# Performance work log

Hardware: AMD Instinct MI355X
Metric: run time of the kernel (lower is better)

Reference implementation:

```python
import math
import jax, jax.numpy as jnp
import numpy as np

B, S, E = 2, 2048, 2048
H, D = 16, 128

def setup_inputs() -> dict:
    key = jax.random.key(0)
    ks = jax.random.split(key, 5)
    scale = 0.02
    return {
        "hidden_states": jax.random.normal(ks[0], (B, S, E), dtype=jnp.float32),
        "Wq": jax.random.normal(ks[1], (E, E), dtype=jnp.float32) * scale,
        "Wk": jax.random.normal(ks[2], (E, E), dtype=jnp.float32) * scale,
        "Wv": jax.random.normal(ks[3], (E, E), dtype=jnp.float32) * scale,
        "Wo": jax.random.normal(ks[4], (E, E), dtype=jnp.float32) * scale,
        "bo": jnp.zeros((E,), dtype=jnp.float32),
    }

def _split_heads(x):
    # [B,S,E] -> [B,H,S,D]
    b, s, _ = x.shape
    return x.reshape(b, s, H, D).transpose(0, 2, 1, 3)

def reference(hidden_states, Wq, Wk, Wv, Wo, bo):
    # torch nn.Linear: y = x @ W.T (q/k/v have no bias)
    q = _split_heads(hidden_states @ Wq.T)
    k = _split_heads(hidden_states @ Wk.T)
    v = _split_heads(hidden_states @ Wv.T)
    scores = jnp.einsum("bhqd,bhkd->bhqk", q, k) / math.sqrt(D)
    # causal mask: strictly-upper-triangular positions set to -inf ...
    causal = jnp.triu(jnp.ones((S, S), dtype=bool), k=1)
    scores = jnp.where(causal[None, None], -jnp.inf, scores)
    # ... then clamped to [-1e4, 1e4] (so masked logits become -10000, not -inf)
    scores = jnp.clip(scores, -10000.0, 10000.0)
    attn = jax.nn.softmax(scores, axis=-1)
    out = jnp.einsum("bhqk,bhkd->bhqd", attn, v)  # [B,H,S,D]
    out = out.transpose(0, 2, 1, 3).reshape(B, S, E)  # merge heads
    return out @ Wo.T + bo
```

## Files before the change

kernel.cpp:

```cpp
#include <hip/hip_runtime.h>
#include <hip/hip_bf16.h>
#include <stdint.h>
#include <math.h>

#define B_ 2
#define S_ 2048
#define E_ 2048
#define H_ 16
#define D_ 128
#define M_ (B_*S_)

typedef _Float16 half8 __attribute__((ext_vector_type(8)));
typedef _Float16 half4 __attribute__((ext_vector_type(4)));
typedef float    floatx4 __attribute__((ext_vector_type(4)));

__device__ __forceinline__ void async_copy16(const void* g, void* lds_base) {
    __builtin_amdgcn_global_load_lds(
        (__attribute__((address_space(1))) void*)(uintptr_t)g,
        (__attribute__((address_space(3))) void*)(uint32_t)(uintptr_t)lds_base,
        16, 0, 0);
}

__global__ __launch_bounds__(256) void cast_all(
    const float* __restrict__ X,  const float* __restrict__ Wq,
    const float* __restrict__ Wk, const float* __restrict__ Wv,
    const float* __restrict__ Wo,
    _Float16* __restrict__ Xh,  _Float16* __restrict__ Wqh,
    _Float16* __restrict__ Wkh, _Float16* __restrict__ Wvh,
    _Float16* __restrict__ Woh)
{
    const int z = blockIdx.z;
    const float* in; _Float16* out; size_t off = 0;
    switch (z) {
        case 0: in = X;  out = Xh;  off = 0;        break;
        case 1: in = X;  out = Xh;  off = 1048576;  break;
        case 2: in = Wq; out = Wqh; break;
        case 3: in = Wk; out = Wkh; break;
        case 4: in = Wv; out = Wvh; break;
        default: in = Wo; out = Woh; break;
    }
    size_t i = off + (size_t)blockIdx.x * 256 + threadIdx.x;
    floatx4 v = ((const floatx4*)in)[i];
    ((half4*)out)[i] = __builtin_convertvector(v, half4);
}

#define GBUF (128*64 + 256*64)

__device__ __forceinline__ void stage512(
    const _Float16* __restrict__ gsrc, int ldk,
    _Float16* lbase, int slot0, int wave, int lane)
{
    int slot = slot0 + wave*64 + lane;
    int row  = slot >> 3;
    int sg   = (slot & 7) ^ (row & 7);
    async_copy16(gsrc + (size_t)row * ldk + sg * 8,
                 lbase + (slot0 + wave*64) * 8);
}

template<bool BIAS, typename OutT, int NW, bool TRV>
__global__ __launch_bounds__(512, 2) void gemm_bt(
    const _Float16* __restrict__ A,
    const _Float16* __restrict__ W0, const _Float16* __restrict__ W1,
    const _Float16* __restrict__ W2,
    OutT* __restrict__ C0, OutT* __restrict__ C1, OutT* __restrict__ C2,
    const float* __restrict__ bias, int M, int N, int K)
{
    const _Float16* W = W0; OutT* C = C0;
    if (NW > 1) {
        if (blockIdx.y == 1) { W = W1; C = C1; }
        else if (blockIdx.y == 2) { W = W2; C = C2; }
    }
    __shared__ __align__(16) _Float16 sm[3 * GBUF];

    const int tid  = threadIdx.x;
    const int lane = tid & 63;
    const int wave = tid >> 6;
    const int wm = wave >> 2, wn = wave & 3;
    const int fr = lane & 15, fg = lane >> 4;

    const int bx = blockIdx.x;
    const int n_tile = bx & 7;
    const int m_tile = bx >> 3;
    const int m0 = m_tile * 128;
    const int n0 = n_tile * 256;

    const int NT = K >> 6;

#pragma unroll
    for (int pt = 0; pt < 2; ++pt) {
        _Float16* ab = &sm[pt * GBUF];
        _Float16* bb = ab + 128*64;
        const _Float16* Ag = A + (size_t)m0 * K + pt*64;
        const _Float16* Wg = W + (size_t)n0 * K + pt*64;
        stage512(Ag, K, ab, 0,    wave, lane);
        stage512(Ag, K, ab, 512,  wave, lane);
        stage512(Wg, K, bb, 0,    wave, lane);
        stage512(Wg, K, bb, 512,  wave, lane);
        stage512(Wg, K, bb, 1024, wave, lane);
        stage512(Wg, K, bb, 1536, wave, lane);
    }

    floatx4 acc[4][4] = {};

    for (int t = 0; t < NT; ++t) {
        if (t + 1 < NT) { __asm__ __volatile__("s_waitcnt vmcnt(6)" ::: "memory"); }
        else            { __asm__ __volatile__("s_waitcnt vmcnt(0)" ::: "memory"); }
        __builtin_amdgcn_sched_barrier(0);
        __builtin_amdgcn_s_barrier();
        __builtin_amdgcn_sched_barrier(0);

        const _Float16* Ab = &sm[(t % 3) * GBUF];
        const _Float16* Bb = Ab + 128*64;
        const bool pf = (t + 2 < NT);
        _Float16* pab = &sm[((t + 2) % 3) * GBUF];
        _Float16* pbb = pab + 128*64;
        const _Float16* pAg = A + (size_t)m0 * K + (t + 2)*64;
        const _Float16* pWg = W + (size_t)n0 * K + (t + 2)*64;

        half8 af[4][2], bf[4][2];
#pragma unroll
        for (int mt = 0; mt < 4; ++mt)
#pragma unroll
            for (int kk = 0; kk < 2; ++kk) {
                int row = wm*64 + mt*16 + fr;
                int g = (kk*4 + fg) ^ (row & 7);
                af[mt][kk] = *(const half8*)&Ab[row*64 + g*8];
            }
#pragma unroll
        for (int nt = 0; nt < 4; ++nt)
#pragma unroll
            for (int kk = 0; kk < 2; ++kk) {
                int row = wn*64 + nt*16 + fr;
                int g = (kk*4 + fg) ^ (row & 7);
                bf[nt][kk] = *(const half8*)&Bb[row*64 + g*8];
            }

        if (pf) {
            stage512(pAg, K, pab, 0,    wave, lane);
            stage512(pAg, K, pab, 512,  wave, lane);
            stage512(pWg, K, pbb, 0,    wave, lane);
            stage512(pWg, K, pbb, 512,  wave, lane);
            stage512(pWg, K, pbb, 1024, wave, lane);
            stage512(pWg, K, pbb, 1536, wave, lane);
        }

        __builtin_amdgcn_s_setprio(1);
#pragma unroll
        for (int kk = 0; kk < 2; ++kk)
#pragma unroll
            for (int nt = 0; nt < 4; ++nt)
#pragma unroll
                for (int mt = 0; mt < 4; ++mt)
                    acc[mt][nt] = __builtin_amdgcn_mfma_f32_16x16x32_f16(
                        af[mt][kk], bf[nt][kk], acc[mt][nt], 0, 0, 0);
        __builtin_amdgcn_s_setprio(0);
    }

    if (TRV && NW > 1 && blockIdx.y == 2) {
        _Float16* Vt = (_Float16*)C;
#pragma unroll
        for (int mt = 0; mt < 4; ++mt)
#pragma unroll
            for (int nt = 0; nt < 4; ++nt) {
                int col  = n0 + wn*64 + nt*16 + fr;
                int row0 = m0 + wm*64 + mt*16 + fg*4;
                int bq = row0 >> 11, s0 = row0 & 2047;
                int hq = col >> 7,  dq = col & 127;
                half4 v;
#pragma unroll
                for (int r = 0; r < 4; ++r) v[r] = (_Float16)acc[mt][nt][r];
                *(half4*)&Vt[(((size_t)(bq*16 + hq) * 128 + dq) << 11) + s0] = v;
            }
    } else {
#pragma unroll
        for (int mt = 0; mt < 4; ++mt)
#pragma unroll
            for (int nt = 0; nt < 4; ++nt) {
                int col = n0 + wn*64 + nt*16 + fr;
                float bv = BIAS ? bias[col] : 0.f;
#pragma unroll
                for (int r = 0; r < 4; ++r) {
                    int row = m0 + wm*64 + mt*16 + fg*4 + r;
                    C[(size_t)row * N + col] = (OutT)(acc[mt][nt][r] + bv);
                }
            }
    }
}

__global__ __launch_bounds__(256, 2) void attn_causal_coop(
    const _Float16* __restrict__ Q, const _Float16* __restrict__ K,
    const _Float16* __restrict__ Vt, _Float16* __restrict__ O)
{
    const int n   = blockIdx.x;
    const int xcd = n & 7;
    const int idx = n >> 3;
    const int bh  = xcd * 4 + (idx >> 4);
    const int j   = idx & 15;
    const int b = bh >> 4, h = bh & 15;
    const int tid = threadIdx.x, lane = tid & 63, wave = tid >> 6;
    const int fr = lane & 15, fg = lane >> 4;

    __shared__ __align__(16) _Float16 Ks[2][64*128];
    __shared__ __align__(16) _Float16 Vs[128*64];
    __shared__ __align__(16) _Float16 Ps[4][32*72];

    const int rhi = (31 - j) * 64 + wave * 16;
    const int rlo = j * 64 + wave * 16;
    const int nkt = 32 - j;

    half8 qf[2][4];
    {
        const _Float16* qb0 = Q + ((size_t)(b*S_) + rhi) * E_ + h*D_;
        const _Float16* qb1 = Q + ((size_t)(b*S_) + rlo) * E_ + h*D_;
#pragma unroll
        for (int kk = 0; kk < 4; ++kk) {
            qf[0][kk] = *(const half8*)&qb0[(size_t)fr * E_ + kk*32 + fg*8];
            qf[1][kk] = *(const half8*)&qb1[(size_t)fr * E_ + kk*32 + fg*8];
        }
    }

    float m_i[2][4], l_i[2][4];
    floatx4 o[2][8] = {};
#pragma unroll
    for (int mt = 0; mt < 2; ++mt)
#pragma unroll
        for (int r = 0; r < 4; ++r) { m_i[mt][r] = -INFINITY; l_i[mt][r] = 0.f; }

    const float scale = 0.088388347648318447f;
    const _Float16* kg = K + (size_t)(b*S_) * E_ + h*D_;
    const _Float16* vg = Vt + (size_t)bh * D_ * S_;
    _Float16* ps = &Ps[wave][0];

#pragma unroll
    for (int q = 0; q < 4; ++q) {
        int G = q*256 + tid;
        int row = G >> 4, slot = G & 15;
        int c = slot ^ (row & 7);
        async_copy16(kg + (size_t)row * E_ + c*8, &Ks[0][(q*256 + wave*64) * 8]);
    }

    for (int jt = 0; jt < nkt; ++jt) {
        __asm__ __volatile__("s_waitcnt vmcnt(0)" ::: "memory");
        __builtin_amdgcn_sched_barrier(0);
        __builtin_amdgcn_s_barrier();
        __builtin_amdgcn_sched_barrier(0);

#pragma unroll
        for (int q = 0; q < 4; ++q) {
            int G = q*256 + tid;
            int row = G >> 3, slot = G & 7;
            int c = slot ^ (row & 7);
            async_copy16(vg + (size_t)row * S_ + jt*64 + c*8,
                         &Vs[(q*256 + wave*64) * 8]);
        }
        const bool pk = (jt + 1 < nkt);
        if (pk) {
#pragma unroll
            for (int q = 0; q < 4; ++q) {
                int G = q*256 + tid;
                int row = G >> 4, slot = G & 15;
                int c = slot ^ (row & 7);
                async_copy16(kg + (size_t)((jt+1)*64 + row) * E_ + c*8,
                             &Ks[(jt+1) & 1][(q*256 + wave*64) * 8]);
            }
        }

        const bool lo_act = (jt <= j);
        const _Float16* kt = &Ks[jt & 1][0];

        floatx4 sacc[2][4] = {};
        __builtin_amdgcn_s_setprio(1);
#pragma unroll
        for (int kk = 0; kk < 4; ++kk) {
            half8 bf[4];
#pragma unroll
            for (int nt = 0; nt < 4; ++nt)
                bf[nt] = *(const half8*)
                    &kt[(nt*16 + fr)*128 + (((kk*4 + fg) ^ (fr & 7)) * 8)];
#pragma unroll
            for (int nt = 0; nt < 4; ++nt)
                sacc[0][nt] = __builtin_amdgcn_mfma_f32_16x16x32_f16(
                    qf[0][kk], bf[nt], sacc[0][nt], 0, 0, 0);
            if (lo_act) {
#pragma unroll
                for (int nt = 0; nt < 4; ++nt)
                    sacc[1][nt] = __builtin_amdgcn_mfma_f32_16x16x32_f16(
                        qf[1][kk], bf[nt], sacc[1][nt], 0, 0, 0);
            }
        }
        __builtin_amdgcn_s_setprio(0);

        const int kc0 = jt*64 + fr;
#pragma unroll
        for (int mt = 0; mt < 2; ++mt) {
            if (mt == 1 && !lo_act) continue;
            const int qr0 = (mt ? rlo : rhi) + fg*4;
            float alpha[4];
#pragma unroll
            for (int r = 0; r < 4; ++r) {
                float mx = -INFINITY;
#pragma unroll
                for (int nt = 0; nt < 4; ++nt) {
                    float s = sacc[mt][nt][r] * scale;
                    s = (kc0 + nt*16 <= qr0 + r) ? s : -INFINITY;
                    sacc[mt][nt][r] = s;
                    mx = fmaxf(mx, s);
                }
                mx = fmaxf(mx, __shfl_xor(mx, 1));
                mx = fmaxf(mx, __shfl_xor(mx, 2));
                mx = fmaxf(mx, __shfl_xor(mx, 4));
                mx = fmaxf(mx, __shfl_xor(mx, 8));
                float mnew = fmaxf(m_i[mt][r], mx);
                alpha[r] = (m_i[mt][r] == -INFINITY) ? 0.f : __expf(m_i[mt][r] - mnew);
                float rs = 0.f;
#pragma unroll
                for (int nt = 0; nt < 4; ++nt) {
                    float p = __expf(sacc[mt][nt][r] - mnew);
                    sacc[mt][nt][r] = p;
                    rs += p;
                }
                rs += __shfl_xor(rs, 1);
                rs += __shfl_xor(rs, 2);
                rs += __shfl_xor(rs, 4);
                rs += __shfl_xor(rs, 8);
                l_i[mt][r] = alpha[r] * l_i[mt][r] + rs;
                m_i[mt][r] = mnew;
            }
#pragma unroll
            for (int dt = 0; dt < 8; ++dt)
#pragma unroll
                for (int r = 0; r < 4; ++r) o[mt][dt][r] *= alpha[r];

#pragma unroll
            for (int nt = 0; nt < 4; ++nt)
#pragma unroll
                for (int r = 0; r < 4; ++r)
                    ps[(mt*16 + fg*4 + r)*72 + nt*16 + fr] = (_Float16)sacc[mt][nt][r];
        }
        __asm__ __volatile__("s_waitcnt lgkmcnt(0)" ::: "memory");
        __builtin_amdgcn_sched_barrier(0);

        if (pk) { __asm__ __volatile__("s_waitcnt vmcnt(4)" ::: "memory"); }
        else    { __asm__ __volatile__("s_waitcnt vmcnt(0)" ::: "memory"); }
        __builtin_amdgcn_sched_barrier(0);
        __builtin_amdgcn_s_barrier();
        __builtin_amdgcn_sched_barrier(0);

        __builtin_amdgcn_s_setprio(1);
#pragma unroll
        for (int kk = 0; kk < 2; ++kk) {
            half8 pf0 = *(const half8*)&ps[(fr)*72 + kk*32 + fg*8];
            half8 pf1 = *(const half8*)&ps[(16 + fr)*72 + kk*32 + fg*8];
#pragma unroll
            for (int dt = 0; dt < 8; ++dt) {
                half8 vf = *(const half8*)
                    &Vs[(dt*16 + fr)*64 + (((kk*4 + fg) ^ (fr & 7)) * 8)];
                o[0][dt] = __builtin_amdgcn_mfma_f32_16x16x32_f16(
                    pf0, vf, o[0][dt], 0, 0, 0);
                if (lo_act)
                    o[1][dt] = __builtin_amdgcn_mfma_f32_16x16x32_f16(
                        pf1, vf, o[1][dt], 0, 0, 0);
            }
        }
        __builtin_amdgcn_s_setprio(0);
    }

#pragma unroll
    for (int mt = 0; mt < 2; ++mt) {
        const int rbase = mt ? rlo : rhi;
        _Float16* ob = O + ((size_t)(b*S_) + rbase) * E_ + h*D_;
#pragma unroll
        for (int r = 0; r < 4; ++r) {
            float inv = 1.f / l_i[mt][r];
#pragma unroll
            for (int dt = 0; dt < 8; ++dt)
                ob[(size_t)(fg*4 + r) * E_ + dt*16 + fr] = (_Float16)(o[mt][dt][r] * inv);
        }
    }
}

extern "C" void kernel_launch(void* const* d_in, const int* in_sizes, int n_in,
                              void* d_out, int out_size, void* d_ws, size_t ws_size,
                              hipStream_t stream) {
    const float* X  = (const float*)d_in[0];
    const float* Wq = (const float*)d_in[1];
    const float* Wk = (const float*)d_in[2];
    const float* Wv = (const float*)d_in[3];
    const float* Wo = (const float*)d_in[4];
    const float* bo = (const float*)d_in[5];
    float* out = (float*)d_out;

    const size_t ME = (size_t)M_ * E_;
    const size_t EE = (size_t)E_ * E_;
    _Float16* ws  = (_Float16*)d_ws;
    _Float16* Xh  = ws;
    _Float16* Wqh = Xh  + ME;
    _Float16* Wkh = Wqh + EE;
    _Float16* Wvh = Wkh + EE;
    _Float16* Woh = Wvh + EE;
    _Float16* Qh  = Woh + EE;
    _Float16* Kh  = Qh  + ME;
    _Float16* Vth = Kh  + ME;
    _Float16* Oh  = Xh;

    cast_all<<<dim3(4096, 1, 6), dim3(256), 0, stream>>>(
        X, Wq, Wk, Wv, Wo, Xh, Wqh, Wkh, Wvh, Woh);

    gemm_bt<false, _Float16, 3, true><<<dim3(256, 3), dim3(512), 0, stream>>>(
        Xh, Wqh, Wkh, Wvh, Qh, Kh, Vth, nullptr, M_, E_, E_);

    attn_causal_coop<<<dim3(512), dim3(256), 0, stream>>>(Qh, Kh, Vth, Oh);

    gemm_bt<true, float, 1, false><<<dim3(256, 1), dim3(512), 0, stream>>>(
        Oh, Woh, nullptr, nullptr, out, nullptr, nullptr, bo, M_, E_, E_);
}
```

Baseline: 400.5 us.

## Fold softmax scale into Q projection, use exp2 and DPP reductions, drop K double-buffer

The Q projection epilogue now multiplies by scale*log2(e), so the attention kernel can use raw v_exp_f32 (exp2) and skip the per-element scale multiply. Masking is applied only on diagonal tiles, and the row max/sum reductions use DPP moves in place of shuffles. The K double-buffer prefetch, the manual waitcnt pipelining and the setprio hints are removed in favour of a single buffer with __syncthreads, which cuts LDS use but exposes load latency each iteration. Storing pre-scaled Q in fp16 changes rounding slightly.

```diff
diff --git a/kernel.cpp b/kernel.cpp
--- a/kernel.cpp
+++ b/kernel.cpp
@@ -10,6 +10,8 @@
 #define D_ 128
 #define M_ (B_*S_)
 
+#define QSCALE 0.1275174308f
+
 typedef _Float16 half8 __attribute__((ext_vector_type(8)));
 typedef _Float16 half4 __attribute__((ext_vector_type(4)));
 typedef float    floatx4 __attribute__((ext_vector_type(4)));
@@ -19,6 +21,29 @@
         (__attribute__((address_space(1))) void*)(uintptr_t)g,
         (__attribute__((address_space(3))) void*)(uint32_t)(uintptr_t)lds_base,
         16, 0, 0);
+}
+
+template<int CTRL>
+__device__ __forceinline__ float dpp_mv(float x) {
+    return __int_as_float(__builtin_amdgcn_update_dpp(
+        0, __float_as_int(x), CTRL, 0xF, 0xF, true));
+}
+__device__ __forceinline__ float row_max16(float x) {
+    x = fmaxf(x, dpp_mv<0xB1>(x));
+    x = fmaxf(x, dpp_mv<0x4E>(x));
+    x = fmaxf(x, dpp_mv<0x124>(x));
+    x = fmaxf(x, dpp_mv<0x128>(x));
+    return x;
+}
+__device__ __forceinline__ float row_sum16(float x) {
+    x += dpp_mv<0xB1>(x);
+    x += dpp_mv<0x4E>(x);
+    x += dpp_mv<0x124>(x);
+    x += dpp_mv<0x128>(x);
+    return x;
+}
+__device__ __forceinline__ float fexp2(float x) {
+    float r; __asm__("v_exp_f32 %0, %1" : "=v"(r) : "v"(x)); return r;
 }
 
 __global__ __launch_bounds__(256) void cast_all(
@@ -172,6 +197,7 @@
                 *(half4*)&Vt[(((size_t)(bq*16 + hq) * 128 + dq) << 11) + s0] = v;
             }
     } else {
+        const float qs = (NW > 1 && blockIdx.y == 0) ? QSCALE : 1.f;
 #pragma unroll
         for (int mt = 0; mt < 4; ++mt)
 #pragma unroll
@@ -181,7 +207,7 @@
 #pragma unroll
                 for (int r = 0; r < 4; ++r) {
                     int row = m0 + wm*64 + mt*16 + fg*4 + r;
-                    C[(size_t)row * N + col] = (OutT)(acc[mt][nt][r] + bv);
+                    C[(size_t)row * N + col] = (OutT)(acc[mt][nt][r] * qs + bv);
                 }
             }
     }
@@ -200,7 +226,7 @@
     const int tid = threadIdx.x, lane = tid & 63, wave = tid >> 6;
     const int fr = lane & 15, fg = lane >> 4;
 
-    __shared__ __align__(16) _Float16 Ks[2][64*128];
+    __shared__ __align__(16) _Float16 Ks[64*128];
     __shared__ __align__(16) _Float16 Vs[128*64];
     __shared__ __align__(16) _Float16 Ps[4][32*72];
 
@@ -226,25 +252,20 @@
 #pragma unroll
         for (int r = 0; r < 4; ++r) { m_i[mt][r] = -INFINITY; l_i[mt][r] = 0.f; }
 
-    const float scale = 0.088388347648318447f;
     const _Float16* kg = K + (size_t)(b*S_) * E_ + h*D_;
     const _Float16* vg = Vt + (size_t)bh * D_ * S_;
     _Float16* ps = &Ps[wave][0];
 
-#pragma unroll
-    for (int q = 0; q < 4; ++q) {
-        int G = q*256 + tid;
-        int row = G >> 4, slot = G & 15;
-        int c = slot ^ (row & 7);
-        async_copy16(kg + (size_t)row * E_ + c*8, &Ks[0][(q*256 + wave*64) * 8]);
-    }
-
     for (int jt = 0; jt < nkt; ++jt) {
-        __asm__ __volatile__("s_waitcnt vmcnt(0)" ::: "memory");
-        __builtin_amdgcn_sched_barrier(0);
-        __builtin_amdgcn_s_barrier();
-        __builtin_amdgcn_sched_barrier(0);
-
+        __syncthreads();
+#pragma unroll
+        for (int q = 0; q < 4; ++q) {
+            int G = q*256 + tid;
+            int row = G >> 4, slot = G & 15;
+            int c = slot ^ (row & 7);
+            async_copy16(kg + (size_t)(jt*64 + row) * E_ + c*8,
+                         &Ks[(q*256 + wave*64) * 8]);
+        }
 #pragma unroll
         for (int q = 0; q < 4; ++q) {
             int G = q*256 + tid;
@@ -253,30 +274,18 @@
             async_copy16(vg + (size_t)row * S_ + jt*64 + c*8,
                          &Vs[(q*256 + wave*64) * 8]);
         }
-        const bool pk = (jt + 1 < nkt);
-        if (pk) {
-#pragma unroll
-            for (int q = 0; q < 4; ++q) {
-                int G = q*256 + tid;
-                int row = G >> 4, slot = G & 15;
-                int c = slot ^ (row & 7);
-                async_copy16(kg + (size_t)((jt+1)*64 + row) * E_ + c*8,
-                             &Ks[(jt+1) & 1][(q*256 + wave*64) * 8]);
-            }
-        }
+        __syncthreads();
 
         const bool lo_act = (jt <= j);
-        const _Float16* kt = &Ks[jt & 1][0];
 
         floatx4 sacc[2][4] = {};
-        __builtin_amdgcn_s_setprio(1);
 #pragma unroll
         for (int kk = 0; kk < 4; ++kk) {
             half8 bf[4];
 #pragma unroll
             for (int nt = 0; nt < 4; ++nt)
                 bf[nt] = *(const half8*)
-                    &kt[(nt*16 + fr)*128 + (((kk*4 + fg) ^ (fr & 7)) * 8)];
+                    &Ks[(nt*16 + fr)*128 + (((kk*4 + fg) ^ (fr & 7)) * 8)];
 #pragma unroll
             for (int nt = 0; nt < 4; ++nt)
                 sacc[0][nt] = __builtin_amdgcn_mfma_f32_16x16x32_f16(
@@ -288,41 +297,41 @@
                         qf[1][kk], bf[nt], sacc[1][nt], 0, 0, 0);
             }
         }
-        __builtin_amdgcn_s_setprio(0);
 
         const int kc0 = jt*64 + fr;
 #pragma unroll
         for (int mt = 0; mt < 2; ++mt) {
             if (mt == 1 && !lo_act) continue;
+            const bool diag = mt ? (jt == j) : (jt == nkt - 1);
             const int qr0 = (mt ? rlo : rhi) + fg*4;
             float alpha[4];
 #pragma unroll
             for (int r = 0; r < 4; ++r) {
-                float mx = -INFINITY;
+                float mx;
+                if (diag) {
+                    mx = -INFINITY;
+#pragma unroll
+                    for (int nt = 0; nt < 4; ++nt) {
+                        float s = sacc[mt][nt][r];
+                        s = (kc0 + nt*16 <= qr0 + r) ? s : -INFINITY;
+                        sacc[mt][nt][r] = s;
+                        mx = fmaxf(mx, s);
+                    }
+                } else {
+                    mx = fmaxf(fmaxf(sacc[mt][0][r], sacc[mt][1][r]),
+                               fmaxf(sacc[mt][2][r], sacc[mt][3][r]));
+                }
+                mx = row_max16(mx);
+                float mnew = fmaxf(m_i[mt][r], mx);
+                alpha[r] = (m_i[mt][r] == -INFINITY) ? 0.f : fexp2(m_i[mt][r] - mnew);
+                float rs = 0.f;
 #pragma unroll
                 for (int nt = 0; nt < 4; ++nt) {
-                    float s = sacc[mt][nt][r] * scale;
-                    s = (kc0 + nt*16 <= qr0 + r) ? s : -INFINITY;
-                    sacc[mt][nt][r] = s;
-                    mx = fmaxf(mx, s);
-                }
-                mx = fmaxf(mx, __shfl_xor(mx, 1));
-                mx = fmaxf(mx, __shfl_xor(mx, 2));
-                mx = fmaxf(mx, __shfl_xor(mx, 4));
-                mx = fmaxf(mx, __shfl_xor(mx, 8));
-                float mnew = fmaxf(m_i[mt][r], mx);
-                alpha[r] = (m_i[mt][r] == -INFINITY) ? 0.f : __expf(m_i[mt][r] - mnew);
-                float rs = 0.f;
-#pragma unroll
-                for (int nt = 0; nt < 4; ++nt) {
-                    float p = __expf(sacc[mt][nt][r] - mnew);
+                    float p = fexp2(sacc[mt][nt][r] - mnew);
                     sacc[mt][nt][r] = p;
                     rs += p;
                 }
-                rs += __shfl_xor(rs, 1);
-                rs += __shfl_xor(rs, 2);
-                rs += __shfl_xor(rs, 4);
-                rs += __shfl_xor(rs, 8);
+                rs = row_sum16(rs);
                 l_i[mt][r] = alpha[r] * l_i[mt][r] + rs;
                 m_i[mt][r] = mnew;
             }
@@ -340,13 +349,6 @@
         __asm__ __volatile__("s_waitcnt lgkmcnt(0)" ::: "memory");
         __builtin_amdgcn_sched_barrier(0);
 
-        if (pk) { __asm__ __volatile__("s_waitcnt vmcnt(4)" ::: "memory"); }
-        else    { __asm__ __volatile__("s_waitcnt vmcnt(0)" ::: "memory"); }
-        __builtin_amdgcn_sched_barrier(0);
-        __builtin_amdgcn_s_barrier();
-        __builtin_amdgcn_sched_barrier(0);
-
-        __builtin_amdgcn_s_setprio(1);
 #pragma unroll
         for (int kk = 0; kk < 2; ++kk) {
             half8 pf0 = *(const half8*)&ps[(fr)*72 + kk*32 + fg*8];
@@ -362,7 +364,6 @@
                         pf1, vf, o[1][dt], 0, 0, 0);
             }
         }
-        __builtin_amdgcn_s_setprio(0);
     }
 
 #pragma unroll
```

New measurement: 381.1 us. 4.8% less time.
